# Optimization experiments

Measured on AMD Instinct MI355X. Metric: run time of the kernel, lower is better.

The kernel has to match this reference:

```python
import jax, jax.numpy as jnp
import numpy as np

BETA = 1e-7

def pearson_corr(x, y):
    # torch.std is Bessel-corrected (ddof=1); corr clamped to [-1,1]
    n = x.shape[-1]
    cx = x - jnp.mean(x, axis=-1, keepdims=True)
    cy = y - jnp.mean(y, axis=-1, keepdims=True)
    cov = jnp.sum(cx * cy, axis=-1, keepdims=True) / (n - 1)
    xs = jnp.std(x, axis=-1, keepdims=True, ddof=1)
    ys = jnp.std(y, axis=-1, keepdims=True, ddof=1)
    return jnp.clip(cov / (xs * ys + BETA), -1.0, 1.0)

def pearson_loss(p, t):
    return jnp.mean(1.0 - pearson_corr(p, t))

def self_cos_sim(x):
    # x: [B,T,C] -> cosine-similarity map [B,T,T]
    num = jnp.einsum('btc,bsc->bts', x, x)
    d = jnp.sqrt(jnp.sum(x * x, axis=-1, keepdims=True))  # [B,T,1]
    den = d @ jnp.swapaxes(d, 1, 2)                        # [B,T,T]
    return num / den

def turn_into_waves(ssm):
    # Assumed Turn_map_into_waves: average SSM rows -> [B,T]
    return jnp.mean(ssm, axis=1)

def psd(x):
    # Assumed FFT_Batch: power spectrum along last dim
    return jnp.abs(jnp.fft.rfft(x, axis=-1)) ** 2

def loss_distill_pyramid(on_ssm, tg_ssm):
    w_on = turn_into_waves(on_ssm)
    w_tg = turn_into_waves(tg_ssm)
    mse = jnp.mean((on_ssm - tg_ssm) ** 2) + jnp.mean((w_on - w_tg) ** 2)
    return mse + pearson_loss(on_ssm, tg_ssm) + pearson_loss(w_on, w_tg)

def loss_reg(ssm):
    # Vectorized replacement of per-diagonal nested loops + torch.std.
    # For offset k in [1, n-2]: std over the k-th superdiagonal (m = n-k
    # elements, Bessel-corrected), scaled by m/20; mean over offsets & batch.
    n = ssm.shape[-1]
    ii, jj = np.triu_indices(n, k=1)
    seg = jj - ii - 1                               # segment = offset-1 in [0, n-2]
    onehot = jax.nn.one_hot(jnp.asarray(seg), n - 1, dtype=ssm.dtype)  # [M, n-1]
    vals = ssm[:, ii, jj]                           # [B, M] upper-tri gather
    s1 = vals @ onehot                              # per-diagonal sums   [B, n-1]
    s2 = (vals * vals) @ onehot                     # per-diagonal sum-sq [B, n-1]
    m = jnp.asarray(n - 1 - np.arange(n - 1), dtype=ssm.dtype)
    var = jnp.where(m > 1, (s2 - s1 * s1 / m) / jnp.maximum(m - 1, 1.0), 0.0)
    std = jnp.sqrt(jnp.maximum(var, 0.0)) * m / 20.0
    return jnp.mean(std[:, : n - 2])                # original drops last diagonal

def loss_freq(ssm):
    waves = turn_into_waves(ssm)
    p = psd(waves)
    L = p.shape[-1]
    lf, hf = int(0.5 * L / 30.0), int(3 * L / 30.0)
    p = p[:, : L // 2]
    p = p / jnp.max(p, axis=-1, keepdims=True)
    return jnp.mean(jnp.sum(p, axis=-1) / jnp.sum(p[:, lf:hf], axis=-1) - 1.0)

def loss_distill_rppg(on, tg):
    temporal = pearson_loss(on, tg)
    L = on.shape[-1]
    lf, hf, vhf = int(0.5 * L / 30.0), int(3 * L / 30.0), int(15 * L / 30.0)
    so = psd(on)[:, :vhf]
    st = psd(tg)[:, :vhf]
    so = so / jnp.max(so, axis=-1, keepdims=True)
    st = st / jnp.max(st, axis=-1, keepdims=True)
    partition = jnp.sum(so, axis=-1) / jnp.sum(so[:, lf:hf], axis=-1) - 1.0
    return temporal + pearson_loss(so, st) + jnp.mean(partition)

def setup_inputs() -> dict:
    key = jax.random.key(0)
    k1, k2, k3, k4 = jax.random.split(key, 4)
    B, T, C, L = 128, 256, 768, 576
    return {
        'pyr_online': jax.random.normal(k1, (B, T, C), dtype=jnp.float32),
        'pyr_target': jax.random.normal(k2, (B, T, C), dtype=jnp.float32),
        'rppg_online': jax.random.normal(k3, (B, L), dtype=jnp.float32),
        'rppg_target': jax.random.normal(k4, (B, L), dtype=jnp.float32),
    }

def reference(pyr_online, pyr_target, rppg_online, rppg_target):
    tg_ssm = self_cos_sim(jax.lax.stop_gradient(pyr_target))
    on_ssm = self_cos_sim(pyr_online)
    loss_pyramid = loss_distill_pyramid(on_ssm, tg_ssm) * 0.5
    loss_r = loss_reg(on_ssm) * 0.5          # single pyramid level (len=1)
    loss_f = loss_freq(on_ssm) * 0.2
    loss_rppg = loss_distill_rppg(rppg_online, jax.lax.stop_gradient(rppg_target)) * 0.5
    total = loss_rppg + loss_pyramid + loss_r + loss_f
    return (total, loss_pyramid, loss_rppg, loss_r, loss_f)
```

## Files before the change

### kernel.cpp

```cpp
#include <hip/hip_runtime.h>
#include <hip/hip_bf16.h>

#define NB 128
#define NT 256
#define NC 768
#define NL 576

constexpr size_t OFF_P1    = 4096;
constexpr size_t OFF_WON   = 135168;
constexpr size_t OFF_WTG   = 167936;
constexpr size_t OFF_PW    = 200704;
constexpr size_t OFF_FRQ   = 200960;
constexpr size_t OFF_RG    = 209280;
constexpr size_t OFF_RPG   = 241920;
constexpr size_t OFF_SO    = 242304;
constexpr size_t OFF_ST    = 279168;
constexpr size_t OFF_SSM_ON_B = (size_t)2 * 1024 * 1024;
constexpr size_t OFF_SSM_TG_B = OFF_SSM_ON_B + (size_t)NB * NT * NT * 2;

typedef __attribute__((ext_vector_type(8))) short short8v;
typedef __attribute__((ext_vector_type(4))) float f32x4;

__device__ __forceinline__ unsigned short f2bf(float f) {
    __hip_bfloat16 h = __float2bfloat16(f);
    unsigned short u; __builtin_memcpy(&u, &h, 2); return u;
}
__device__ __forceinline__ float bf2f(unsigned short u) {
    __hip_bfloat16 h; __builtin_memcpy(&h, &u, 2); return __bfloat162float(h);
}

__device__ __forceinline__ float sin2pi(float x) {
    x -= floorf(x + 0.5f);
    float x2 = x * x;
    float p = 3.8199526f;
    p = p * x2 - 15.094643f;
    p = p * x2 + 42.058693f;
    p = p * x2 - 76.705860f;
    p = p * x2 + 81.605249f;
    p = p * x2 - 41.341702f;
    p = p * x2 + 6.2831853f;
    return p * x;
}
__device__ __forceinline__ float cos2pi(float x) { return sin2pi(x + 0.25f); }

__device__ __forceinline__ float blockSum(float v, float* tmp) {
    int lane = threadIdx.x & 63, wid = threadIdx.x >> 6;
#pragma unroll
    for (int o = 32; o; o >>= 1) v += __shfl_down(v, o, 64);
    __syncthreads();
    if (lane == 0) tmp[wid] = v;
    __syncthreads();
    return tmp[0] + tmp[1] + tmp[2] + tmp[3];
}
__device__ __forceinline__ float blockMax(float v, float* tmp) {
    int lane = threadIdx.x & 63, wid = threadIdx.x >> 6;
#pragma unroll
    for (int o = 32; o; o >>= 1) v = fmaxf(v, __shfl_down(v, o, 64));
    __syncthreads();
    if (lane == 0) tmp[wid] = v;
    __syncthreads();
    return fmaxf(fmaxf(tmp[0], tmp[1]), fmaxf(tmp[2], tmp[3]));
}
__device__ __forceinline__ float pearson1m(float S0, float S1, float S2, float S3,
                                           float S4, float n) {
    float cov = (S4 - S0 * S1 / n) / (n - 1.f);
    float xs = sqrtf(fmaxf((S2 - S0 * S0 / n) / (n - 1.f), 0.f));
    float ys = sqrtf(fmaxf((S3 - S1 * S1 / n) / (n - 1.f), 0.f));
    float corr = fminf(1.f, fmaxf(-1.f, cov / (xs * ys + 1e-7f)));
    return 1.f - corr;
}

#define ROWSTR 40
#define LDS_HALF7 (128 * ROWSTR)
__global__ __launch_bounds__(256) void gram7_k(const float* __restrict__ on,
                                               const float* __restrict__ tg,
                                               unsigned short* __restrict__ ssm_on,
                                               unsigned short* __restrict__ ssm_tg) {
    __shared__ unsigned short lds[2 * LDS_HALF7];
    __shared__ float invs[128];
    int lin = blockIdx.x;
    int xcd = lin & 7, m = lin >> 3;
    int pair = (m >> 4) * 8 + xcd;
    int tile = m & 15;
    int rt = tile >> 2, ct = tile & 3;
    int b = pair >> 1, tau = pair & 1;
    const float* X = tau ? tg : on;
    unsigned short* S = (tau ? ssm_tg : ssm_on) + (size_t)b * NT * NT;

    int t = threadIdx.x;
    int wave = t >> 6, lane = t & 63;
    int fr = lane & 15, fq = lane >> 4;
    int wr = (wave >> 1) * 32, wc = (wave & 1) * 32;

    int rl = t >> 1, h = t & 1;
    int grow = (rl < 64) ? (rt * 64 + rl) : (ct * 64 + (rl - 64));
    const float* src = X + ((size_t)b * NT + grow) * NC + h * 16;
    int stoff = rl * ROWSTR + h * 16;
    float sq = 0.f;

    int offA0 = (wr + fr) * ROWSTR + 8 * fq;
    int offA1 = (wr + 16 + fr) * ROWSTR + 8 * fq;
    int offB0 = (64 + wc + fr) * ROWSTR + 8 * fq;
    int offB1 = (64 + wc + 16 + fr) * ROWSTR + 8 * fq;

    f32x4 acc[2][2] = {};

    {
        float4 a = *reinterpret_cast<const float4*>(src);
        float4 bb = *reinterpret_cast<const float4*>(src + 4);
        float4 cc = *reinterpret_cast<const float4*>(src + 8);
        float4 d = *reinterpret_cast<const float4*>(src + 12);
        sq += a.x * a.x + a.y * a.y + a.z * a.z + a.w * a.w;
        sq += bb.x * bb.x + bb.y * bb.y + bb.z * bb.z + bb.w * bb.w;
        sq += cc.x * cc.x + cc.y * cc.y + cc.z * cc.z + cc.w * cc.w;
        sq += d.x * d.x + d.y * d.y + d.z * d.z + d.w * d.w;
        short8v v0, v1;
        v0[0] = (short)f2bf(a.x); v0[1] = (short)f2bf(a.y);
        v0[2] = (short)f2bf(a.z); v0[3] = (short)f2bf(a.w);
        v0[4] = (short)f2bf(bb.x); v0[5] = (short)f2bf(bb.y);
        v0[6] = (short)f2bf(bb.z); v0[7] = (short)f2bf(bb.w);
        v1[0] = (short)f2bf(cc.x); v1[1] = (short)f2bf(cc.y);
        v1[2] = (short)f2bf(cc.z); v1[3] = (short)f2bf(cc.w);
        v1[4] = (short)f2bf(d.x); v1[5] = (short)f2bf(d.y);
        v1[6] = (short)f2bf(d.z); v1[7] = (short)f2bf(d.w);
        *reinterpret_cast<short8v*>(&lds[stoff]) = v0;
        *reinterpret_cast<short8v*>(&lds[stoff + 8]) = v1;
    }
    __syncthreads();

    int cur = 0;
#pragma unroll 1
    for (int s = 0; s < 24; s++) {
        unsigned short* rb = &lds[cur * LDS_HALF7];
        short8v A0 = *reinterpret_cast<short8v*>(rb + offA0);
        short8v A1 = *reinterpret_cast<short8v*>(rb + offA1);
        short8v B0 = *reinterpret_cast<short8v*>(rb + offB0);
        short8v B1 = *reinterpret_cast<short8v*>(rb + offB1);
        float4 a, bb, cc, d;
        if (s < 23) {
            const float* p = src + 32 * (s + 1);
            a = *reinterpret_cast<const float4*>(p);
            bb = *reinterpret_cast<const float4*>(p + 4);
            cc = *reinterpret_cast<const float4*>(p + 8);
            d = *reinterpret_cast<const float4*>(p + 12);
        }
        acc[0][0] = __builtin_amdgcn_mfma_f32_16x16x32_bf16(A0, B0, acc[0][0], 0, 0, 0);
        acc[0][1] = __builtin_amdgcn_mfma_f32_16x16x32_bf16(A0, B1, acc[0][1], 0, 0, 0);
        acc[1][0] = __builtin_amdgcn_mfma_f32_16x16x32_bf16(A1, B0, acc[1][0], 0, 0, 0);
        acc[1][1] = __builtin_amdgcn_mfma_f32_16x16x32_bf16(A1, B1, acc[1][1], 0, 0, 0);
        if (s < 23) {
            unsigned short* wbuf = &lds[(cur ^ 1) * LDS_HALF7];
            sq += a.x * a.x + a.y * a.y + a.z * a.z + a.w * a.w;
            sq += bb.x * bb.x + bb.y * bb.y + bb.z * bb.z + bb.w * bb.w;
            sq += cc.x * cc.x + cc.y * cc.y + cc.z * cc.z + cc.w * cc.w;
            sq += d.x * d.x + d.y * d.y + d.z * d.z + d.w * d.w;
            short8v v0, v1;
            v0[0] = (short)f2bf(a.x); v0[1] = (short)f2bf(a.y);
            v0[2] = (short)f2bf(a.z); v0[3] = (short)f2bf(a.w);
            v0[4] = (short)f2bf(bb.x); v0[5] = (short)f2bf(bb.y);
            v0[6] = (short)f2bf(bb.z); v0[7] = (short)f2bf(bb.w);
            v1[0] = (short)f2bf(cc.x); v1[1] = (short)f2bf(cc.y);
            v1[2] = (short)f2bf(cc.z); v1[3] = (short)f2bf(cc.w);
            v1[4] = (short)f2bf(d.x); v1[5] = (short)f2bf(d.y);
            v1[6] = (short)f2bf(d.z); v1[7] = (short)f2bf(d.w);
            *reinterpret_cast<short8v*>(wbuf + stoff) = v0;
            *reinterpret_cast<short8v*>(wbuf + stoff + 8) = v1;
        }
        __syncthreads();
        cur ^= 1;
    }
    {
        float v = sq + __shfl_xor(sq, 1, 64);
        if (h == 0) invs[rl] = 1.f / sqrtf(v);
    }
    __syncthreads();
#pragma unroll
    for (int f = 0; f < 2; f++) {
        int rowl = wr + 16 * f + 4 * fq;
#pragma unroll
        for (int g = 0; g < 2; g++) {
            int coll = wc + 16 * g + fr;
            float ic = invs[64 + coll];
            int gcol = ct * 64 + coll;
#pragma unroll
            for (int r = 0; r < 4; r++)
                S[(size_t)(rt * 64 + rowl + r) * NT + gcol] =
                    f2bf(acc[f][g][r] * invs[rowl + r] * ic);
        }
    }
}

__global__ __launch_bounds__(256) void pearson256w_k(const unsigned short* __restrict__ A,
                                                     const unsigned short* __restrict__ Bv,
                                                     float* __restrict__ part,
                                                     float* __restrict__ won,
                                                     float* __restrict__ wtg) {
    size_t base = (size_t)blockIdx.x * NT;
    int tid = threadIdx.x;
    int lane = tid & 63, wid = tid >> 6;
    float o = bf2f(A[base + tid]), g = bf2f(Bv[base + tid]);
    float v6[6] = {o, g, o * o, g * g, o * g, (o - g) * (o - g)};
    __shared__ float tmp[4][6];
#pragma unroll
    for (int j = 0; j < 6; j++) {
        float x = v6[j];
#pragma unroll
        for (int off = 32; off; off >>= 1) x += __shfl_down(x, off, 64);
        v6[j] = x;
    }
    if (lane == 0) {
#pragma unroll
        for (int j = 0; j < 6; j++) tmp[wid][j] = v6[j];
    }
    __syncthreads();
    if (tid == 0) {
        float S[6];
#pragma unroll
        for (int j = 0; j < 6; j++)
            S[j] = tmp[0][j] + tmp[1][j] + tmp[2][j] + tmp[3][j];
        part[2 * blockIdx.x + 0] = pearson1m(S[0], S[1], S[2], S[3], S[4], 256.f);
        part[2 * blockIdx.x + 1] = S[5];
        won[blockIdx.x] = S[0] * (1.f / NT);
        wtg[blockIdx.x] = S[1] * (1.f / NT);
    }
}

__global__ __launch_bounds__(256) void pearsonW_k(const float* __restrict__ A,
                                                  const float* __restrict__ Bv,
                                                  float* __restrict__ part) {
    size_t base = (size_t)blockIdx.x * NT;
    int tid = threadIdx.x;
    float o = A[base + tid], g = Bv[base + tid];
    __shared__ float tmp[4];
    float S0 = blockSum(o, tmp);
    float S1 = blockSum(g, tmp);
    float S2 = blockSum(o * o, tmp);
    float S3 = blockSum(g * g, tmp);
    float S4 = blockSum(o * g, tmp);
    float S5 = blockSum((o - g) * (o - g), tmp);
    if (tid == 0) {
        part[2 * blockIdx.x + 0] = pearson1m(S0, S1, S2, S3, S4, 256.f);
        part[2 * blockIdx.x + 1] = S5;
    }
}

__global__ __launch_bounds__(256) void freqbin_k(const float* __restrict__ w,
                                                 float* __restrict__ frq) {
    int k = blockIdx.x, b = blockIdx.y, m = threadIdx.x;
    float val = w[b * NT + m];
    float x = (float)((m * k) & 255) * (1.f / 256.f);
    __shared__ float tmp[4];
    float re = blockSum(val * cos2pi(x), tmp);
    float im = blockSum(val * sin2pi(x), tmp);
    if (m == 0) frq[b * 64 + k] = re * re + im * im;
}

__global__ __launch_bounds__(256) void regdiag_k(const unsigned short* __restrict__ ssm,
                                                 float* __restrict__ rg) {
    int d = blockIdx.x + 1, b = blockIdx.y, i = threadIdx.x;
    int col = i + d;
    bool ok = col < 256;
    float v = 0.f;
    if (ok) v = bf2f(ssm[(size_t)b * NT * NT + i * NT + col]);
    __shared__ float tmp[4];
    float s1 = blockSum(v, tmp);
    float s2 = blockSum(v * v, tmp);
    if (i == 0) {
        float outv = 0.f;
        if (d <= 254) {
            float mm = (float)(256 - d);
            float var = (s2 - s1 * s1 / mm) / (mm - 1.f);
            outv = sqrtf(fmaxf(var, 0.f)) * mm * 0.05f;
        }
        rg[b * 255 + (d - 1)] = outv;
    }
}

__global__ __launch_bounds__(256) void rppgbin_k(const float* __restrict__ on,
                                                 const float* __restrict__ tg,
                                                 float* __restrict__ so,
                                                 float* __restrict__ st,
                                                 float* __restrict__ tq) {
    int k = blockIdx.x, b = blockIdx.y, t = threadIdx.x;
    const float* po = on + (size_t)b * NL;
    const float* pg = tg + (size_t)b * NL;
    float o1 = po[t], g1 = pg[t];
    float o2 = po[t + 256], g2 = pg[t + 256];
    bool h3 = t < 64;
    float o3 = h3 ? po[t + 512] : 0.f, g3 = h3 ? pg[t + 512] : 0.f;
    __shared__ float tmp[4];
    if (k == 0) {
        float S0 = blockSum(o1 + o2 + o3, tmp);
        float S1 = blockSum(g1 + g2 + g3, tmp);
        float S2 = blockSum(o1 * o1 + o2 * o2 + o3 * o3, tmp);
        float S3 = blockSum(g1 * g1 + g2 * g2 + g3 * g3, tmp);
        float S4 = blockSum(o1 * g1 + o2 * g2 + o3 * g3, tmp);
        if (t == 0) tq[3 * b + 0] = pearson1m(S0, S1, S2, S3, S4, 576.f);
        __syncthreads();
    }
    float reo, imo, reg_, img;
    {
        float x1 = (float)((t * k) % NL) * (1.f / 576.f);
        float c1 = cos2pi(x1), s1 = sin2pi(x1);
        float x2 = (float)(((t + 256) * k) % NL) * (1.f / 576.f);
        float c2 = cos2pi(x2), s2 = sin2pi(x2);
        reo = o1 * c1 + o2 * c2; imo = o1 * s1 + o2 * s2;
        reg_ = g1 * c1 + g2 * c2; img = g1 * s1 + g2 * s2;
        if (h3) {
            float x3 = (float)(((t + 512) * k) % NL) * (1.f / 576.f);
            float c3 = cos2pi(x3), s3 = sin2pi(x3);
            reo = fmaf(o3, c3, reo); imo = fmaf(o3, s3, imo);
            reg_ = fmaf(g3, c3, reg_); img = fmaf(g3, s3, img);
        }
    }
    float RO = blockSum(reo, tmp);
    float IO = blockSum(imo, tmp);
    float RG = blockSum(reg_, tmp);
    float IG = blockSum(img, tmp);
    if (t == 0) {
        so[b * 288 + k] = RO * RO + IO * IO;
        st[b * 288 + k] = RG * RG + IG * IG;
    }
}

__global__ __launch_bounds__(256) void rppgfin_k(const float* __restrict__ so,
                                                 const float* __restrict__ st,
                                                 float* __restrict__ tq) {
    int b = blockIdx.x, t = threadIdx.x;
    const float* SO = so + (size_t)b * 288;
    const float* ST = st + (size_t)b * 288;
    float a0 = SO[t], b0 = ST[t];
    bool h2 = t < 32;
    float a1 = h2 ? SO[t + 256] : 0.f, b1 = h2 ? ST[t + 256] : 0.f;
    __shared__ float tmp[4];
    float Mo = blockMax(fmaxf(a0, a1), tmp);
    float Mg = blockMax(fmaxf(b0, b1), tmp);
    if (Mo <= 0.f) Mo = 1.f;
    if (Mg <= 0.f) Mg = 1.f;
    float n0 = a0 / Mo, m0 = b0 / Mg;
    float n1 = a1 / Mo, m1 = b1 / Mg;
    float S0 = blockSum(n0 + n1, tmp);
    float S1 = blockSum(m0 + m1, tmp);
    float S2 = blockSum(n0 * n0 + n1 * n1, tmp);
    float S3 = blockSum(m0 * m0 + m1 * m1, tmp);
    float S4 = blockSum(n0 * m0 + n1 * m1, tmp);
    float bt0 = (t >= 9 && t < 57) ? a0 : 0.f;
    float TT = blockSum(a0 + a1, tmp);
    float TB = blockSum(bt0, tmp);
    if (t == 0) {
        tq[3 * b + 1] = pearson1m(S0, S1, S2, S3, S4, 288.f);
        tq[3 * b + 2] = (TB > 0.f) ? (TT / TB - 1.f) : 0.f;
    }
}

__global__ __launch_bounds__(256) void final_k(const float* __restrict__ ws,
                                               float* __restrict__ out) {
    __shared__ float tmp[4];
    int tid = threadIdx.x;
    const float* p1 = ws + OFF_P1;
    float a = 0.f, bsum = 0.f;
    for (int i = tid; i < 32768; i += 256) { a += p1[2 * i]; bsum += p1[2 * i + 1]; }
    float S0 = blockSum(a, tmp);
    float S1 = blockSum(bsum, tmp);
    const float* pw = ws + OFF_PW;
    float c0 = 0.f, c1 = 0.f;
    for (int i = tid; i < 128; i += 256) { c0 += pw[2 * i]; c1 += pw[2 * i + 1]; }
    float W0 = blockSum(c0, tmp);
    float W1 = blockSum(c1, tmp);
    const float* frq = ws + OFF_FRQ;
    float fqv = 0.f;
    if (tid < 128) {
        float Ft = 0.f, Fb = 0.f;
        for (int k = 0; k < 64; k++) {
            float v = frq[tid * 64 + k];
            Ft += v;
            if (k >= 2 && k < 12) Fb += v;
        }
        if (Fb > 0.f) fqv = Ft / Fb - 1.f;
    }
    float Fq = blockSum(fqv, tmp);
    const float* rg = ws + OFF_RG;
    float e = 0.f;
    for (int i = tid; i < 32640; i += 256) e += rg[i];
    float Rg = blockSum(e, tmp);
    const float* tq = ws + OFF_RPG;
    float g0 = 0.f, g1 = 0.f, g2 = 0.f;
    for (int i = tid; i < 128; i += 256) {
        g0 += tq[3 * i]; g1 += tq[3 * i + 1]; g2 += tq[3 * i + 2];
    }
    float R0 = blockSum(g0, tmp);
    float R1 = blockSum(g1, tmp);
    float R2 = blockSum(g2, tmp);
    if (tid == 0) {
        float loss_pyr  = 0.5f * (S1 / 8388608.f + W1 / 32768.f + S0 / 32768.f + W0 / 128.f);
        float loss_r    = 0.5f * Rg / (128.f * 254.f);
        float loss_f    = 0.2f * Fq / 128.f;
        float loss_rppg = 0.5f * (R0 + R1 + R2) / 128.f;
        float total = loss_rppg + loss_pyr + loss_r + loss_f;
        out[0] = total;
        out[1] = loss_pyr;
        out[2] = loss_rppg;
        out[3] = loss_r;
        out[4] = loss_f;
    }
}

extern "C" void kernel_launch(void* const* d_in, const int* in_sizes, int n_in,
                              void* d_out, int out_size, void* d_ws, size_t ws_size,
                              hipStream_t stream) {
    const float* pyr_on  = (const float*)d_in[0];
    const float* pyr_tg  = (const float*)d_in[1];
    const float* rppg_on = (const float*)d_in[2];
    const float* rppg_tg = (const float*)d_in[3];
    float* ws = (float*)d_ws;
    unsigned short* ssm_on = (unsigned short*)((char*)d_ws + OFF_SSM_ON_B);
    unsigned short* ssm_tg = (unsigned short*)((char*)d_ws + OFF_SSM_TG_B);
    float* out = (float*)d_out;

    gram7_k<<<4096, 256, 0, stream>>>(pyr_on, pyr_tg, ssm_on, ssm_tg);
    pearson256w_k<<<32768, 256, 0, stream>>>(ssm_on, ssm_tg, ws + OFF_P1,
                                             ws + OFF_WON, ws + OFF_WTG);
    pearsonW_k<<<NB, 256, 0, stream>>>(ws + OFF_WON, ws + OFF_WTG, ws + OFF_PW);
    freqbin_k<<<dim3(64, NB), 256, 0, stream>>>(ws + OFF_WON, ws + OFF_FRQ);
    regdiag_k<<<dim3(255, NB), 256, 0, stream>>>(ssm_on, ws + OFF_RG);
    rppgbin_k<<<dim3(288, NB), 256, 0, stream>>>(rppg_on, rppg_tg,
                                                 ws + OFF_SO, ws + OFF_ST, ws + OFF_RPG);
    rppgfin_k<<<NB, 256, 0, stream>>>(ws + OFF_SO, ws + OFF_ST, ws + OFF_RPG);
    final_k<<<1, 256, 0, stream>>>(ws, out);
}
```

Measured before the change: 311.7 us.

## Merge independent post-gram kernels into two block-dispatched mega kernels

Seven small reduction kernels that run after the Gram matrix are merged into two launches. Each launch picks its role from the block index: rPPG DFT bins, row Pearson and diagonal std in the first; frequency bins, wave Pearson and rPPG final in the second. This removes launch gaps and tail idle time between dependent small kernels. It also changes the LDS row stride in the gram kernel from 40 to 36, which alters bank-conflict behaviour and could add conflicts.

New measurement: 452.9 us. +45.3%, slower.

```diff
diff --git a/kernel.cpp b/kernel.cpp
--- a/kernel.cpp
+++ b/kernel.cpp
@@ -70,13 +70,13 @@
     return 1.f - corr;
 }
 
-#define ROWSTR 40
-#define LDS_HALF7 (128 * ROWSTR)
-__global__ __launch_bounds__(256) void gram7_k(const float* __restrict__ on,
+#define ROWSTR 36
+#define LDS_HALF8 (128 * ROWSTR)
+__global__ __launch_bounds__(256) void gram8_k(const float* __restrict__ on,
                                                const float* __restrict__ tg,
                                                unsigned short* __restrict__ ssm_on,
                                                unsigned short* __restrict__ ssm_tg) {
-    __shared__ unsigned short lds[2 * LDS_HALF7];
+    __shared__ unsigned short lds[2 * LDS_HALF8];
     __shared__ float invs[128];
     int lin = blockIdx.x;
     int xcd = lin & 7, m = lin >> 3;
@@ -131,7 +131,7 @@
     int cur = 0;
 #pragma unroll 1
     for (int s = 0; s < 24; s++) {
-        unsigned short* rb = &lds[cur * LDS_HALF7];
+        unsigned short* rb = &lds[cur * LDS_HALF8];
         short8v A0 = *reinterpret_cast<short8v*>(rb + offA0);
         short8v A1 = *reinterpret_cast<short8v*>(rb + offA1);
         short8v B0 = *reinterpret_cast<short8v*>(rb + offB0);
@@ -149,7 +149,7 @@
         acc[1][0] = __builtin_amdgcn_mfma_f32_16x16x32_bf16(A1, B0, acc[1][0], 0, 0, 0);
         acc[1][1] = __builtin_amdgcn_mfma_f32_16x16x32_bf16(A1, B1, acc[1][1], 0, 0, 0);
         if (s < 23) {
-            unsigned short* wbuf = &lds[(cur ^ 1) * LDS_HALF7];
+            unsigned short* wbuf = &lds[(cur ^ 1) * LDS_HALF8];
             sq += a.x * a.x + a.y * a.y + a.z * a.z + a.w * a.w;
             sq += bb.x * bb.x + bb.y * bb.y + bb.z * bb.z + bb.w * bb.w;
             sq += cc.x * cc.x + cc.y * cc.y + cc.z * cc.z + cc.w * cc.w;
@@ -190,166 +190,153 @@
     }
 }
 
-__global__ __launch_bounds__(256) void pearson256w_k(const unsigned short* __restrict__ A,
-                                                     const unsigned short* __restrict__ Bv,
-                                                     float* __restrict__ part,
-                                                     float* __restrict__ won,
-                                                     float* __restrict__ wtg) {
-    size_t base = (size_t)blockIdx.x * NT;
-    int tid = threadIdx.x;
-    int lane = tid & 63, wid = tid >> 6;
-    float o = bf2f(A[base + tid]), g = bf2f(Bv[base + tid]);
-    float v6[6] = {o, g, o * o, g * g, o * g, (o - g) * (o - g)};
-    __shared__ float tmp[4][6];
-#pragma unroll
-    for (int j = 0; j < 6; j++) {
-        float x = v6[j];
-#pragma unroll
-        for (int off = 32; off; off >>= 1) x += __shfl_down(x, off, 64);
-        v6[j] = x;
-    }
-    if (lane == 0) {
-#pragma unroll
-        for (int j = 0; j < 6; j++) tmp[wid][j] = v6[j];
-    }
-    __syncthreads();
-    if (tid == 0) {
-        float S[6];
-#pragma unroll
-        for (int j = 0; j < 6; j++)
-            S[j] = tmp[0][j] + tmp[1][j] + tmp[2][j] + tmp[3][j];
-        part[2 * blockIdx.x + 0] = pearson1m(S[0], S[1], S[2], S[3], S[4], 256.f);
-        part[2 * blockIdx.x + 1] = S[5];
-        won[blockIdx.x] = S[0] * (1.f / NT);
-        wtg[blockIdx.x] = S[1] * (1.f / NT);
-    }
-}
-
-__global__ __launch_bounds__(256) void pearsonW_k(const float* __restrict__ A,
-                                                  const float* __restrict__ Bv,
-                                                  float* __restrict__ part) {
-    size_t base = (size_t)blockIdx.x * NT;
-    int tid = threadIdx.x;
-    float o = A[base + tid], g = Bv[base + tid];
+__global__ __launch_bounds__(256) void mega1_k(const float* __restrict__ rppg_on,
+                                               const float* __restrict__ rppg_tg,
+                                               const unsigned short* __restrict__ ssm_on,
+                                               const unsigned short* __restrict__ ssm_tg,
+                                               float* __restrict__ ws) {
+    __shared__ float tmp6[4][6];
+    float* tmp = &tmp6[0][0];
+    int bid = blockIdx.x, t = threadIdx.x;
+    int lane = t & 63, wid = t >> 6;
+
+    if (bid < 36864) {
+        int k = bid % 288, b = bid / 288;
+        const float* po = rppg_on + (size_t)b * NL;
+        const float* pg = rppg_tg + (size_t)b * NL;
+        float o1 = po[t], g1 = pg[t];
+        float o2 = po[t + 256], g2 = pg[t + 256];
+        bool h3 = t < 64;
+        float o3 = h3 ? po[t + 512] : 0.f, g3 = h3 ? pg[t + 512] : 0.f;
+        if (k == 0) {
+            float S0 = blockSum(o1 + o2 + o3, tmp);
+            float S1 = blockSum(g1 + g2 + g3, tmp);
+            float S2 = blockSum(o1 * o1 + o2 * o2 + o3 * o3, tmp);
+            float S3 = blockSum(g1 * g1 + g2 * g2 + g3 * g3, tmp);
+            float S4 = blockSum(o1 * g1 + o2 * g2 + o3 * g3, tmp);
+            if (t == 0) ws[OFF_RPG + 3 * b + 0] = pearson1m(S0, S1, S2, S3, S4, 576.f);
+            __syncthreads();
+        }
+        float reo, imo, reg_, img;
+        {
+            float x1 = (float)((t * k) % NL) * (1.f / 576.f);
+            float c1 = cos2pi(x1), s1 = sin2pi(x1);
+            float x2 = (float)(((t + 256) * k) % NL) * (1.f / 576.f);
+            float c2 = cos2pi(x2), s2 = sin2pi(x2);
+            reo = o1 * c1 + o2 * c2; imo = o1 * s1 + o2 * s2;
+            reg_ = g1 * c1 + g2 * c2; img = g1 * s1 + g2 * s2;
+            if (h3) {
+                float x3 = (float)(((t + 512) * k) % NL) * (1.f / 576.f);
+                float c3 = cos2pi(x3), s3 = sin2pi(x3);
+                reo = fmaf(o3, c3, reo); imo = fmaf(o3, s3, imo);
+                reg_ = fmaf(g3, c3, reg_); img = fmaf(g3, s3, img);
+            }
+        }
+        float RO = blockSum(reo, tmp);
+        float IO = blockSum(imo, tmp);
+        float RG = blockSum(reg_, tmp);
+        float IG = blockSum(img, tmp);
+        if (t == 0) {
+            ws[OFF_SO + b * 288 + k] = RO * RO + IO * IO;
+            ws[OFF_ST + b * 288 + k] = RG * RG + IG * IG;
+        }
+    } else if (bid < 69632) {
+        int row = bid - 36864;
+        size_t base = (size_t)row * NT;
+        float o = bf2f(ssm_on[base + t]), g = bf2f(ssm_tg[base + t]);
+        float v6[6] = {o, g, o * o, g * g, o * g, (o - g) * (o - g)};
+#pragma unroll
+        for (int j = 0; j < 6; j++) {
+            float x = v6[j];
+#pragma unroll
+            for (int off = 32; off; off >>= 1) x += __shfl_down(x, off, 64);
+            v6[j] = x;
+        }
+        if (lane == 0) {
+#pragma unroll
+            for (int j = 0; j < 6; j++) tmp6[wid][j] = v6[j];
+        }
+        __syncthreads();
+        if (t == 0) {
+            float S[6];
+#pragma unroll
+            for (int j = 0; j < 6; j++)
+                S[j] = tmp6[0][j] + tmp6[1][j] + tmp6[2][j] + tmp6[3][j];
+            ws[OFF_P1 + 2 * row + 0] = pearson1m(S[0], S[1], S[2], S[3], S[4], 256.f);
+            ws[OFF_P1 + 2 * row + 1] = S[5];
+            ws[OFF_WON + row] = S[0] * (1.f / NT);
+            ws[OFF_WTG + row] = S[1] * (1.f / NT);
+        }
+    } else {
+        int q = bid - 69632;
+        int b = q / 255, d = q % 255 + 1;
+        int col = t + d;
+        bool ok = col < 256;
+        float v = 0.f;
+        if (ok) v = bf2f(ssm_on[(size_t)b * NT * NT + t * NT + col]);
+        float s1 = blockSum(v, tmp);
+        float s2 = blockSum(v * v, tmp);
+        if (t == 0) {
+            float outv = 0.f;
+            if (d <= 254) {
+                float mm = (float)(256 - d);
+                float var = (s2 - s1 * s1 / mm) / (mm - 1.f);
+                outv = sqrtf(fmaxf(var, 0.f)) * mm * 0.05f;
+            }
+            ws[OFF_RG + b * 255 + (d - 1)] = outv;
+        }
+    }
+}
+
+__global__ __launch_bounds__(256) void mega2_k(float* __restrict__ ws) {
     __shared__ float tmp[4];
-    float S0 = blockSum(o, tmp);
-    float S1 = blockSum(g, tmp);
-    float S2 = blockSum(o * o, tmp);
-    float S3 = blockSum(g * g, tmp);
-    float S4 = blockSum(o * g, tmp);
-    float S5 = blockSum((o - g) * (o - g), tmp);
-    if (tid == 0) {
-        part[2 * blockIdx.x + 0] = pearson1m(S0, S1, S2, S3, S4, 256.f);
-        part[2 * blockIdx.x + 1] = S5;
-    }
-}
-
-__global__ __launch_bounds__(256) void freqbin_k(const float* __restrict__ w,
-                                                 float* __restrict__ frq) {
-    int k = blockIdx.x, b = blockIdx.y, m = threadIdx.x;
-    float val = w[b * NT + m];
-    float x = (float)((m * k) & 255) * (1.f / 256.f);
-    __shared__ float tmp[4];
-    float re = blockSum(val * cos2pi(x), tmp);
-    float im = blockSum(val * sin2pi(x), tmp);
-    if (m == 0) frq[b * 64 + k] = re * re + im * im;
-}
-
-__global__ __launch_bounds__(256) void regdiag_k(const unsigned short* __restrict__ ssm,
-                                                 float* __restrict__ rg) {
-    int d = blockIdx.x + 1, b = blockIdx.y, i = threadIdx.x;
-    int col = i + d;
-    bool ok = col < 256;
-    float v = 0.f;
-    if (ok) v = bf2f(ssm[(size_t)b * NT * NT + i * NT + col]);
-    __shared__ float tmp[4];
-    float s1 = blockSum(v, tmp);
-    float s2 = blockSum(v * v, tmp);
-    if (i == 0) {
-        float outv = 0.f;
-        if (d <= 254) {
-            float mm = (float)(256 - d);
-            float var = (s2 - s1 * s1 / mm) / (mm - 1.f);
-            outv = sqrtf(fmaxf(var, 0.f)) * mm * 0.05f;
-        }
-        rg[b * 255 + (d - 1)] = outv;
-    }
-}
-
-__global__ __launch_bounds__(256) void rppgbin_k(const float* __restrict__ on,
-                                                 const float* __restrict__ tg,
-                                                 float* __restrict__ so,
-                                                 float* __restrict__ st,
-                                                 float* __restrict__ tq) {
-    int k = blockIdx.x, b = blockIdx.y, t = threadIdx.x;
-    const float* po = on + (size_t)b * NL;
-    const float* pg = tg + (size_t)b * NL;
-    float o1 = po[t], g1 = pg[t];
-    float o2 = po[t + 256], g2 = pg[t + 256];
-    bool h3 = t < 64;
-    float o3 = h3 ? po[t + 512] : 0.f, g3 = h3 ? pg[t + 512] : 0.f;
-    __shared__ float tmp[4];
-    if (k == 0) {
-        float S0 = blockSum(o1 + o2 + o3, tmp);
-        float S1 = blockSum(g1 + g2 + g3, tmp);
-        float S2 = blockSum(o1 * o1 + o2 * o2 + o3 * o3, tmp);
-        float S3 = blockSum(g1 * g1 + g2 * g2 + g3 * g3, tmp);
-        float S4 = blockSum(o1 * g1 + o2 * g2 + o3 * g3, tmp);
-        if (t == 0) tq[3 * b + 0] = pearson1m(S0, S1, S2, S3, S4, 576.f);
-        __syncthreads();
-    }
-    float reo, imo, reg_, img;
-    {
-        float x1 = (float)((t * k) % NL) * (1.f / 576.f);
-        float c1 = cos2pi(x1), s1 = sin2pi(x1);
-        float x2 = (float)(((t + 256) * k) % NL) * (1.f / 576.f);
-        float c2 = cos2pi(x2), s2 = sin2pi(x2);
-        reo = o1 * c1 + o2 * c2; imo = o1 * s1 + o2 * s2;
-        reg_ = g1 * c1 + g2 * c2; img = g1 * s1 + g2 * s2;
-        if (h3) {
-            float x3 = (float)(((t + 512) * k) % NL) * (1.f / 576.f);
-            float c3 = cos2pi(x3), s3 = sin2pi(x3);
-            reo = fmaf(o3, c3, reo); imo = fmaf(o3, s3, imo);
-            reg_ = fmaf(g3, c3, reg_); img = fmaf(g3, s3, img);
-        }
-    }
-    float RO = blockSum(reo, tmp);
-    float IO = blockSum(imo, tmp);
-    float RG = blockSum(reg_, tmp);
-    float IG = blockSum(img, tmp);
-    if (t == 0) {
-        so[b * 288 + k] = RO * RO + IO * IO;
-        st[b * 288 + k] = RG * RG + IG * IG;
-    }
-}
-
-__global__ __launch_bounds__(256) void rppgfin_k(const float* __restrict__ so,
-                                                 const float* __restrict__ st,
-                                                 float* __restrict__ tq) {
-    int b = blockIdx.x, t = threadIdx.x;
-    const float* SO = so + (size_t)b * 288;
-    const float* ST = st + (size_t)b * 288;
-    float a0 = SO[t], b0 = ST[t];
-    bool h2 = t < 32;
-    float a1 = h2 ? SO[t + 256] : 0.f, b1 = h2 ? ST[t + 256] : 0.f;
-    __shared__ float tmp[4];
-    float Mo = blockMax(fmaxf(a0, a1), tmp);
-    float Mg = blockMax(fmaxf(b0, b1), tmp);
-    if (Mo <= 0.f) Mo = 1.f;
-    if (Mg <= 0.f) Mg = 1.f;
-    float n0 = a0 / Mo, m0 = b0 / Mg;
-    float n1 = a1 / Mo, m1 = b1 / Mg;
-    float S0 = blockSum(n0 + n1, tmp);
-    float S1 = blockSum(m0 + m1, tmp);
-    float S2 = blockSum(n0 * n0 + n1 * n1, tmp);
-    float S3 = blockSum(m0 * m0 + m1 * m1, tmp);
-    float S4 = blockSum(n0 * m0 + n1 * m1, tmp);
-    float bt0 = (t >= 9 && t < 57) ? a0 : 0.f;
-    float TT = blockSum(a0 + a1, tmp);
-    float TB = blockSum(bt0, tmp);
-    if (t == 0) {
-        tq[3 * b + 1] = pearson1m(S0, S1, S2, S3, S4, 288.f);
-        tq[3 * b + 2] = (TB > 0.f) ? (TT / TB - 1.f) : 0.f;
+    int bid = blockIdx.x, t = threadIdx.x;
+
+    if (bid < 8192) {
+        int k = bid & 63, b = bid >> 6;
+        float val = ws[OFF_WON + b * NT + t];
+        float x = (float)((t * k) & 255) * (1.f / 256.f);
+        float re = blockSum(val * cos2pi(x), tmp);
+        float im = blockSum(val * sin2pi(x), tmp);
+        if (t == 0) ws[OFF_FRQ + b * 64 + k] = re * re + im * im;
+    } else if (bid < 8320) {
+        int b = bid - 8192;
+        float o = ws[OFF_WON + b * NT + t], g = ws[OFF_WTG + b * NT + t];
+        float S0 = blockSum(o, tmp);
+        float S1 = blockSum(g, tmp);
+        float S2 = blockSum(o * o, tmp);
+        float S3 = blockSum(g * g, tmp);
+        float S4 = blockSum(o * g, tmp);
+        float S5 = blockSum((o - g) * (o - g), tmp);
+        if (t == 0) {
+            ws[OFF_PW + 2 * b + 0] = pearson1m(S0, S1, S2, S3, S4, 256.f);
+            ws[OFF_PW + 2 * b + 1] = S5;
+        }
+    } else {
+        int b = bid - 8320;
+        const float* SO = ws + OFF_SO + (size_t)b * 288;
+        const float* ST = ws + OFF_ST + (size_t)b * 288;
+        float a0 = SO[t], b0 = ST[t];
+        bool h2 = t < 32;
+        float a1 = h2 ? SO[t + 256] : 0.f, b1 = h2 ? ST[t + 256] : 0.f;
+        float Mo = blockMax(fmaxf(a0, a1), tmp);
+        float Mg = blockMax(fmaxf(b0, b1), tmp);
+        if (Mo <= 0.f) Mo = 1.f;
+        if (Mg <= 0.f) Mg = 1.f;
+        float n0 = a0 / Mo, m0 = b0 / Mg;
+        float n1 = a1 / Mo, m1 = b1 / Mg;
+        float S0 = blockSum(n0 + n1, tmp);
+        float S1 = blockSum(m0 + m1, tmp);
+        float S2 = blockSum(n0 * n0 + n1 * n1, tmp);
+        float S3 = blockSum(m0 * m0 + m1 * m1, tmp);
+        float S4 = blockSum(n0 * m0 + n1 * m1, tmp);
+        float bt0 = (t >= 9 && t < 57) ? a0 : 0.f;
+        float TT = blockSum(a0 + a1, tmp);
+        float TB = blockSum(bt0, tmp);
+        if (t == 0) {
+            ws[OFF_RPG + 3 * b + 1] = pearson1m(S0, S1, S2, S3, S4, 288.f);
+            ws[OFF_RPG + 3 * b + 2] = (TB > 0.f) ? (TT / TB - 1.f) : 0.f;
+        }
     }
 }
 
@@ -417,14 +404,8 @@
     unsigned short* ssm_tg = (unsigned short*)((char*)d_ws + OFF_SSM_TG_B);
     float* out = (float*)d_out;
 
-    gram7_k<<<4096, 256, 0, stream>>>(pyr_on, pyr_tg, ssm_on, ssm_tg);
-    pearson256w_k<<<32768, 256, 0, stream>>>(ssm_on, ssm_tg, ws + OFF_P1,
-                                             ws + OFF_WON, ws + OFF_WTG);
-    pearsonW_k<<<NB, 256, 0, stream>>>(ws + OFF_WON, ws + OFF_WTG, ws + OFF_PW);
-    freqbin_k<<<dim3(64, NB), 256, 0, stream>>>(ws + OFF_WON, ws + OFF_FRQ);
-    regdiag_k<<<dim3(255, NB), 256, 0, stream>>>(ssm_on, ws + OFF_RG);
-    rppgbin_k<<<dim3(288, NB), 256, 0, stream>>>(rppg_on, rppg_tg,
-                                                 ws + OFF_SO, ws + OFF_ST, ws + OFF_RPG);
-    rppgfin_k<<<NB, 256, 0, stream>>>(ws + OFF_SO, ws + OFF_ST, ws + OFF_RPG);
+    gram8_k<<<4096, 256, 0, stream>>>(pyr_on, pyr_tg, ssm_on, ssm_tg);
+    mega1_k<<<102272, 256, 0, stream>>>(rppg_on, rppg_tg, ssm_on, ssm_tg, ws);
+    mega2_k<<<8448, 256, 0, stream>>>(ws);
     final_k<<<1, 256, 0, stream>>>(ws, out);
 }
```
